# Performance work log

Measured on AMD Instinct MI355X. Metric: run time of the kernel, lower is better.

## Reference

```python
import jax, jax.numpy as jnp
import numpy as np

LAMBDA = 1.0          # lambda_param
SIGMA = 1.0           # RBF bandwidth (sigkernel convention: exp(-||x-y||^2 / sigma))
DYADIC_ORDER = 2
F = 2 ** DYADIC_ORDER # dyadic refinement factor per time axis

B, M_POP, DIM, SEQ_LEN = 4, 16, 8, 65


def _rbf_gram(X, Y):
    # X: (m, L, d), Y: (n, L, d) -> static kernel Gram (m, n, L, L)
    sx = jnp.sum(X * X, -1)                       # (m, L)
    sy = jnp.sum(Y * Y, -1)                       # (n, L)
    inner = jnp.einsum('isd,jtd->ijst', X, Y)     # (m, n, L, L)
    d2 = sx[:, None, :, None] + sy[None, :, None, :] - 2.0 * inner
    return jnp.exp(-d2 / SIGMA)


def _increments(G):
    # double increment of the static Gram over time, then dyadic refinement
    inc = G[..., 1:, 1:] + G[..., :-1, :-1] - G[..., 1:, :-1] - G[..., :-1, 1:]
    inc = jnp.repeat(jnp.repeat(inc, F, axis=-2), F, axis=-1) / (F * F)
    return inc  # (..., S, S) with S = F*(L-1)


def _solve_pde(M):
    # Goursat PDE explicit finite-difference scheme (as in sigkernel):
    # K[i+1,j+1] = (K[i+1,j]+K[i,j+1])*(1 + m/2 + m^2/12) - K[i,j]*(1 - m^2/12)
    dtype = M.dtype
    S = M.shape[0]

    def row_step(prev_row, m_row):
        def cell(k_left, inp):
            k00, k01, m = inp
            a = 1.0 + 0.5 * m + m * m * (1.0 / 12.0)
            b = 1.0 - m * m * (1.0 / 12.0)
            k_new = (k_left + k01) * a - k00 * b
            return k_new, k_new
        _, tail = jax.lax.scan(cell, jnp.asarray(1.0, dtype),
                               (prev_row[:-1], prev_row[1:], m_row))
        new_row = jnp.concatenate([jnp.ones((1,), dtype), tail])
        return new_row, None

    row0 = jnp.ones((S + 1,), dtype)
    last_row, _ = jax.lax.scan(row_step, row0, M)
    return last_row[-1]


def _gram_sig(X, Y):
    # signature kernel Gram matrix: X (m,L,d), Y (n,L,d) -> (m,n)
    Minc = _increments(_rbf_gram(X, Y))
    return jax.vmap(jax.vmap(_solve_pde))(Minc)


def setup_inputs() -> dict:
    key = jax.random.key(0)
    k1, k2 = jax.random.split(key)
    generated_samples = jax.random.normal(k1, (B, M_POP, DIM, SEQ_LEN), dtype=jnp.float32)
    real_sample = jax.random.normal(k2, (B, DIM, SEQ_LEN), dtype=jnp.float32)
    return {"generated_samples": generated_samples, "real_sample": real_sample}


def reference(generated_samples, real_sample):
    # generated_samples: (B, m, dim, L); real_sample: (B, dim, L)
    gen = jnp.swapaxes(generated_samples, -1, -2)          # (B, m, L, d)
    real = jnp.swapaxes(real_sample, -1, -2)[:, None]      # (B, 1, L, d)
    m = gen.shape[1]
    K_XX = jax.vmap(_gram_sig)(gen, gen)                   # (B, m, m)
    K_XY = jax.vmap(_gram_sig)(gen, real)                  # (B, m, 1)
    self_sim = (jnp.sum(K_XX, axis=(-1, -2))
                - jnp.trace(K_XX, axis1=-2, axis2=-1)) / (m * (m - 1))
    cross_sim = jnp.mean(K_XY, axis=(-1, -2))
    return jnp.mean(LAMBDA / 2.0 * self_sim - cross_sim)
```

## Files before the change

### kernel.cpp

```cpp
#include <hip/hip_runtime.h>


#define SEQ   65
#define DIMS  8
#define MPOP  16
#define NBATCH 4
#define NPAIR_XX 120
#define NBLOCKS (NBATCH*(NPAIR_XX + MPOP))
#define MST 67

__device__ __forceinline__ float wave_shr1(float x) {
    int xi = __builtin_bit_cast(int, x);
    int r  = __builtin_amdgcn_update_dpp(xi, xi, 0x138, 0xF, 0xF, false);
    return __builtin_bit_cast(float, r);
}
__device__ __forceinline__ float wave_shl1(float x) {
    int xi = __builtin_bit_cast(int, x);
    int r  = __builtin_amdgcn_update_dpp(xi, xi, 0x130, 0xF, 0xF, false);
    return __builtin_bit_cast(float, r);
}
__device__ __forceinline__ int clamp63(int v) {
    return v < 0 ? 0 : (v > 63 ? 63 : v);
}

__global__ __launch_bounds__(64, 1) void sigker_kernel(
    const float* __restrict__ gen,
    const float* __restrict__ realp,
    float* __restrict__ ws)
{
    __shared__ __align__(16) float YsF[SEQ * DIMS];
    __shared__ float R64[SEQ];
    __shared__ float MmL[64 * MST];

    const int tid = threadIdx.x;
    const int I   = tid;
    const int bid = blockIdx.x;

    int b, ii, jj; bool cross;
    if (bid < NBATCH * NPAIR_XX) {
        b = bid / NPAIR_XX;
        int p = bid % NPAIR_XX;
        int i = 0, acc = 0;
        while (p >= acc + (MPOP - 1 - i)) { acc += (MPOP - 1 - i); ++i; }
        ii = i; jj = i + 1 + (p - acc); cross = false;
    } else {
        int t = bid - NBATCH * NPAIR_XX;
        b = t / MPOP; ii = t % MPOP; jj = 0; cross = true;
    }

    const float* Xg = gen + (size_t)(b * MPOP + ii) * (DIMS * SEQ);
    const float* Yg = cross ? (realp + (size_t)b * (DIMS * SEQ))
                            : (gen + (size_t)(b * MPOP + jj) * (DIMS * SEQ));

    for (int f = tid; f < SEQ * DIMS; f += 64) {
        int d = f / SEQ, s = f - d * SEQ;
        YsF[s * DIMS + d] = Yg[f];
    }
    float x0[DIMS], x64[DIMS];
    #pragma unroll
    for (int d = 0; d < DIMS; ++d) {
        x0[d]  = Xg[d * SEQ + I];
        x64[d] = Xg[d * SEQ + 64];
    }
    __syncthreads();

    for (int t = tid; t < SEQ; t += 64) {
        const float4* yv = (const float4*)&YsF[t * DIMS];
        float4 ya = yv[0], yb = yv[1];
        float dd = 0.f;
        float a0;
        a0 = x64[0]-ya.x; dd += a0*a0;  a0 = x64[1]-ya.y; dd += a0*a0;
        a0 = x64[2]-ya.z; dd += a0*a0;  a0 = x64[3]-ya.w; dd += a0*a0;
        a0 = x64[4]-yb.x; dd += a0*a0;  a0 = x64[5]-yb.y; dd += a0*a0;
        a0 = x64[6]-yb.z; dd += a0*a0;  a0 = x64[7]-yb.w; dd += a0*a0;
        R64[t] = __expf(-dd);
    }
    __syncthreads();

    float* mrow = &MmL[I * MST];
    float ep, enp;
    {
        const float4* yv = (const float4*)&YsF[0];
        float4 ya = yv[0], yb = yv[1];
        float dd = 0.f, a0;
        a0 = x0[0]-ya.x; dd += a0*a0;  a0 = x0[1]-ya.y; dd += a0*a0;
        a0 = x0[2]-ya.z; dd += a0*a0;  a0 = x0[3]-ya.w; dd += a0*a0;
        a0 = x0[4]-yb.x; dd += a0*a0;  a0 = x0[5]-yb.y; dd += a0*a0;
        a0 = x0[6]-yb.z; dd += a0*a0;  a0 = x0[7]-yb.w; dd += a0*a0;
        float e  = __expf(-dd);
        float en = wave_shl1(e);
        float r  = R64[0];
        en = (I == 63) ? r : en;
        ep = e; enp = en;
    }
    #pragma unroll 4
    for (int t = 1; t < SEQ; ++t) {
        const float4* yv = (const float4*)&YsF[t * DIMS];
        float4 ya = yv[0], yb = yv[1];
        float dd = 0.f, a0;
        a0 = x0[0]-ya.x; dd += a0*a0;  a0 = x0[1]-ya.y; dd += a0*a0;
        a0 = x0[2]-ya.z; dd += a0*a0;  a0 = x0[3]-ya.w; dd += a0*a0;
        a0 = x0[4]-yb.x; dd += a0*a0;  a0 = x0[5]-yb.y; dd += a0*a0;
        a0 = x0[6]-yb.z; dd += a0*a0;  a0 = x0[7]-yb.w; dd += a0*a0;
        float e  = __expf(-dd);
        float en = wave_shl1(e);
        float r  = R64[t];
        en = (I == 63) ? r : en;
        mrow[t - 1] = ((en + ep) - (enp + e)) * (1.0f / 16.0f);
        ep = e; enp = en;
    }

    float l0 = 1.f, l1 = 1.f, l2 = 1.f, l3 = 1.f;
    float b0 = 1.f, b1 = 1.f, b2 = 1.f, b3 = 1.f;
    float cnext = 1.f;

#define STEP(DTv, MV) do {                                              \
        float t0_ = wave_shr1(b0);                                      \
        float t1_ = wave_shr1(b1);                                      \
        float t2_ = wave_shr1(b2);                                      \
        float t3_ = wave_shr1(b3);                                      \
        float cc_ = cnext; cnext = t3_;                                 \
        if (I == 0) { t0_ = t1_ = t2_ = t3_ = 1.f; cc_ = 1.f; }         \
        int J_ = (DTv) - I;                                             \
        if ((unsigned)J_ < 64u) {                                       \
            if (J_ == 0) cc_ = 1.f;                                     \
            float m_   = (MV);                                          \
            float q12_ = m_ * m_ * (1.0f / 12.0f);                      \
            float a_   = 1.0f + 0.5f * m_ + q12_;                       \
            float nb_  = q12_ - 1.0f;                                   \
            float u0_ = a_ * t0_ + nb_ * cc_;                           \
            float u1_ = a_ * t1_ + nb_ * t0_;                           \
            float u2_ = a_ * t2_ + nb_ * t1_;                           \
            float u3_ = a_ * t3_ + nb_ * t2_;                           \
            float q1_ = a_ * l0 + u0_;                                  \
            float q2_ = a_ * q1_ + u1_;                                 \
            float q3_ = a_ * q2_ + u2_;                                 \
            float q4_ = a_ * q3_ + u3_;                                 \
            u0_ = a_ * q1_ + nb_ * l0;  u1_ = a_ * q2_ + nb_ * q1_;     \
            u2_ = a_ * q3_ + nb_ * q2_; u3_ = a_ * q4_ + nb_ * q3_;     \
            float r1_ = a_ * l1 + u0_;                                  \
            float r2_ = a_ * r1_ + u1_;                                 \
            float r3_ = a_ * r2_ + u2_;                                 \
            float r4_ = a_ * r3_ + u3_;                                 \
            u0_ = a_ * r1_ + nb_ * l1;  u1_ = a_ * r2_ + nb_ * r1_;     \
            u2_ = a_ * r3_ + nb_ * r2_; u3_ = a_ * r4_ + nb_ * r3_;     \
            float s1_ = a_ * l2 + u0_;                                  \
            float s2_ = a_ * s1_ + u1_;                                 \
            float s3_ = a_ * s2_ + u2_;                                 \
            float s4_ = a_ * s3_ + u3_;                                 \
            u0_ = a_ * s1_ + nb_ * l2;  u1_ = a_ * s2_ + nb_ * s1_;     \
            u2_ = a_ * s3_ + nb_ * s2_; u3_ = a_ * s4_ + nb_ * s3_;     \
            float v1_ = a_ * l3 + u0_;                                  \
            float v2_ = a_ * v1_ + u1_;                                 \
            float v3_ = a_ * v2_ + u2_;                                 \
            float v4_ = a_ * v3_ + u3_;                                 \
            b0 = v1_; b1 = v2_; b2 = v3_; b3 = v4_;                     \
            l0 = q4_; l1 = r4_; l2 = s4_; l3 = v4_;                     \
        }                                                               \
    } while (0)

    float m0 = mrow[clamp63(0 - I)];
    float m1 = mrow[clamp63(1 - I)];
    float m2 = mrow[clamp63(2 - I)];
    float m3 = mrow[clamp63(3 - I)];

    for (int g = 0; g < 32; ++g) {
        const int DT0 = g * 4;
        float n0 = mrow[clamp63(DT0 + 4 - I)];
        float n1 = mrow[clamp63(DT0 + 5 - I)];
        float n2 = mrow[clamp63(DT0 + 6 - I)];
        float n3 = mrow[clamp63(DT0 + 7 - I)];
        STEP(DT0 + 0, m0);
        STEP(DT0 + 1, m1);
        STEP(DT0 + 2, m2);
        STEP(DT0 + 3, m3);
        m0 = n0; m1 = n1; m2 = n2; m3 = n3;
    }
#undef STEP

    if (tid == 63) {
        float w = cross ? (-1.0f / 32.0f) : (1.0f / 480.0f);
        ws[bid] = w * b3;
    }
}

__global__ __launch_bounds__(64, 1) void sigker_reduce(
    const float* __restrict__ ws, float* __restrict__ out)
{
    const int lane = threadIdx.x;
    float s = 0.f;
    for (int k = lane; k < NBLOCKS; k += 64) s += ws[k];
    #pragma unroll
    for (int off = 32; off >= 1; off >>= 1) s += __shfl_xor(s, off);
    if (lane == 0) out[0] = s;
}

extern "C" void kernel_launch(void* const* d_in, const int* in_sizes, int n_in,
                              void* d_out, int out_size, void* d_ws, size_t ws_size,
                              hipStream_t stream) {
    const float* gen   = (const float*)d_in[0];
    const float* realp = (const float*)d_in[1];
    if (n_in >= 2 && in_sizes[0] == NBATCH * DIMS * SEQ) {
        gen   = (const float*)d_in[1];
        realp = (const float*)d_in[0];
    }
    float* ws  = (float*)d_ws;
    float* out = (float*)d_out;
    sigker_kernel<<<NBLOCKS, 64, 0, stream>>>(gen, realp, ws);
    sigker_reduce<<<1, 64, 0, stream>>>(ws, out);
}
```

Baseline: 90.09 us.

## Remove branch from PDE wavefront via zero-padded skewed M layout

Stores each lane's increment row in a zero-padded, skewed shared buffer so the wavefront loop can read m with a fixed stride. This removes the per-step bounds check and the clamp indexing. Out-of-range cells see m=0, which makes the update act as identity on the boundary values. The loop becomes 127 unconditional steps with 8-deep prefetch. It also rewrites the RBF distance as norms minus twice the dot product, and adds a shared-memory zeroing pass plus a larger LDS footprint.

```diff
diff --git a/kernel.cpp b/kernel.cpp
--- a/kernel.cpp
+++ b/kernel.cpp
@@ -7,7 +7,7 @@
 #define NBATCH 4
 #define NPAIR_XX 120
 #define NBLOCKS (NBATCH*(NPAIR_XX + MPOP))
-#define MST 67
+#define MROW  194
 
 __device__ __forceinline__ float wave_shr1(float x) {
     int xi = __builtin_bit_cast(int, x);
@@ -18,9 +18,6 @@
     int xi = __builtin_bit_cast(int, x);
     int r  = __builtin_amdgcn_update_dpp(xi, xi, 0x130, 0xF, 0xF, false);
     return __builtin_bit_cast(float, r);
-}
-__device__ __forceinline__ int clamp63(int v) {
-    return v < 0 ? 0 : (v > 63 ? 63 : v);
 }
 
 __global__ __launch_bounds__(64, 1) void sigker_kernel(
@@ -30,11 +27,22 @@
 {
     __shared__ __align__(16) float YsF[SEQ * DIMS];
     __shared__ float R64[SEQ];
-    __shared__ float MmL[64 * MST];
+    __shared__ float YnL[SEQ];
+    __shared__ __align__(16) float MmL[64 * MROW];
 
     const int tid = threadIdx.x;
     const int I   = tid;
+    const bool lane0 = (I == 0);
     const int bid = blockIdx.x;
+
+    {
+        float4 z4 = make_float4(0.f, 0.f, 0.f, 0.f);
+        float4* M4 = (float4*)MmL;
+        #pragma unroll
+        for (int k = 0; k < (64 * MROW) / 4 / 64; ++k)
+            M4[k * 64 + tid] = z4;
+        if (tid < 32) M4[48 * 64 + tid] = z4;
+    }
 
     int b, ii, jj; bool cross;
     if (bid < NBATCH * NPAIR_XX) {
@@ -57,125 +65,115 @@
         YsF[s * DIMS + d] = Yg[f];
     }
     float x0[DIMS], x64[DIMS];
+    float xn0 = 0.f, xn64 = 0.f;
     #pragma unroll
     for (int d = 0; d < DIMS; ++d) {
         x0[d]  = Xg[d * SEQ + I];
         x64[d] = Xg[d * SEQ + 64];
+        xn0  += x0[d]  * x0[d];
+        xn64 += x64[d] * x64[d];
     }
     __syncthreads();
 
     for (int t = tid; t < SEQ; t += 64) {
         const float4* yv = (const float4*)&YsF[t * DIMS];
         float4 ya = yv[0], yb = yv[1];
-        float dd = 0.f;
-        float a0;
-        a0 = x64[0]-ya.x; dd += a0*a0;  a0 = x64[1]-ya.y; dd += a0*a0;
-        a0 = x64[2]-ya.z; dd += a0*a0;  a0 = x64[3]-ya.w; dd += a0*a0;
-        a0 = x64[4]-yb.x; dd += a0*a0;  a0 = x64[5]-yb.y; dd += a0*a0;
-        a0 = x64[6]-yb.z; dd += a0*a0;  a0 = x64[7]-yb.w; dd += a0*a0;
-        R64[t] = __expf(-dd);
+        float yn  = ya.x*ya.x + ya.y*ya.y + ya.z*ya.z + ya.w*ya.w
+                  + yb.x*yb.x + yb.y*yb.y + yb.z*yb.z + yb.w*yb.w;
+        float dot = x64[0]*ya.x + x64[1]*ya.y + x64[2]*ya.z + x64[3]*ya.w
+                  + x64[4]*yb.x + x64[5]*yb.y + x64[6]*yb.z + x64[7]*yb.w;
+        YnL[t] = yn;
+        R64[t] = __expf(2.f*dot - xn64 - yn);
     }
     __syncthreads();
 
-    float* mrow = &MmL[I * MST];
+    float* mrowW = &MmL[I * MROW + 64];
     float ep, enp;
     {
         const float4* yv = (const float4*)&YsF[0];
         float4 ya = yv[0], yb = yv[1];
-        float dd = 0.f, a0;
-        a0 = x0[0]-ya.x; dd += a0*a0;  a0 = x0[1]-ya.y; dd += a0*a0;
-        a0 = x0[2]-ya.z; dd += a0*a0;  a0 = x0[3]-ya.w; dd += a0*a0;
-        a0 = x0[4]-yb.x; dd += a0*a0;  a0 = x0[5]-yb.y; dd += a0*a0;
-        a0 = x0[6]-yb.z; dd += a0*a0;  a0 = x0[7]-yb.w; dd += a0*a0;
-        float e  = __expf(-dd);
+        float dot = x0[0]*ya.x + x0[1]*ya.y + x0[2]*ya.z + x0[3]*ya.w
+                  + x0[4]*yb.x + x0[5]*yb.y + x0[6]*yb.z + x0[7]*yb.w;
+        float e  = __expf(2.f*dot - xn0 - YnL[0]);
         float en = wave_shl1(e);
-        float r  = R64[0];
-        en = (I == 63) ? r : en;
+        en = (I == 63) ? R64[0] : en;
         ep = e; enp = en;
     }
     #pragma unroll 4
     for (int t = 1; t < SEQ; ++t) {
         const float4* yv = (const float4*)&YsF[t * DIMS];
         float4 ya = yv[0], yb = yv[1];
-        float dd = 0.f, a0;
-        a0 = x0[0]-ya.x; dd += a0*a0;  a0 = x0[1]-ya.y; dd += a0*a0;
-        a0 = x0[2]-ya.z; dd += a0*a0;  a0 = x0[3]-ya.w; dd += a0*a0;
-        a0 = x0[4]-yb.x; dd += a0*a0;  a0 = x0[5]-yb.y; dd += a0*a0;
-        a0 = x0[6]-yb.z; dd += a0*a0;  a0 = x0[7]-yb.w; dd += a0*a0;
-        float e  = __expf(-dd);
+        float dot = x0[0]*ya.x + x0[1]*ya.y + x0[2]*ya.z + x0[3]*ya.w
+                  + x0[4]*yb.x + x0[5]*yb.y + x0[6]*yb.z + x0[7]*yb.w;
+        float e  = __expf(2.f*dot - xn0 - YnL[t]);
         float en = wave_shl1(e);
-        float r  = R64[t];
-        en = (I == 63) ? r : en;
-        mrow[t - 1] = ((en + ep) - (enp + e)) * (1.0f / 16.0f);
+        en = (I == 63) ? R64[t] : en;
+        mrowW[t - 1] = ((en - enp) + (ep - e)) * (1.0f / 16.0f);
         ep = e; enp = en;
     }
 
+    const float* mpde = &MmL[193 * I + 64];
     float l0 = 1.f, l1 = 1.f, l2 = 1.f, l3 = 1.f;
     float b0 = 1.f, b1 = 1.f, b2 = 1.f, b3 = 1.f;
     float cnext = 1.f;
 
-#define STEP(DTv, MV) do {                                              \
+#define STEP(MV) do {                                                   \
         float t0_ = wave_shr1(b0);                                      \
         float t1_ = wave_shr1(b1);                                      \
         float t2_ = wave_shr1(b2);                                      \
         float t3_ = wave_shr1(b3);                                      \
+        if (lane0) { t0_ = 1.f; t1_ = 1.f; t2_ = 1.f; t3_ = 1.f; }      \
         float cc_ = cnext; cnext = t3_;                                 \
-        if (I == 0) { t0_ = t1_ = t2_ = t3_ = 1.f; cc_ = 1.f; }         \
-        int J_ = (DTv) - I;                                             \
-        if ((unsigned)J_ < 64u) {                                       \
-            if (J_ == 0) cc_ = 1.f;                                     \
-            float m_   = (MV);                                          \
-            float q12_ = m_ * m_ * (1.0f / 12.0f);                      \
-            float a_   = 1.0f + 0.5f * m_ + q12_;                       \
-            float nb_  = q12_ - 1.0f;                                   \
-            float u0_ = a_ * t0_ + nb_ * cc_;                           \
-            float u1_ = a_ * t1_ + nb_ * t0_;                           \
-            float u2_ = a_ * t2_ + nb_ * t1_;                           \
-            float u3_ = a_ * t3_ + nb_ * t2_;                           \
-            float q1_ = a_ * l0 + u0_;                                  \
-            float q2_ = a_ * q1_ + u1_;                                 \
-            float q3_ = a_ * q2_ + u2_;                                 \
-            float q4_ = a_ * q3_ + u3_;                                 \
-            u0_ = a_ * q1_ + nb_ * l0;  u1_ = a_ * q2_ + nb_ * q1_;     \
-            u2_ = a_ * q3_ + nb_ * q2_; u3_ = a_ * q4_ + nb_ * q3_;     \
-            float r1_ = a_ * l1 + u0_;                                  \
-            float r2_ = a_ * r1_ + u1_;                                 \
-            float r3_ = a_ * r2_ + u2_;                                 \
-            float r4_ = a_ * r3_ + u3_;                                 \
-            u0_ = a_ * r1_ + nb_ * l1;  u1_ = a_ * r2_ + nb_ * r1_;     \
-            u2_ = a_ * r3_ + nb_ * r2_; u3_ = a_ * r4_ + nb_ * r3_;     \
-            float s1_ = a_ * l2 + u0_;                                  \
-            float s2_ = a_ * s1_ + u1_;                                 \
-            float s3_ = a_ * s2_ + u2_;                                 \
-            float s4_ = a_ * s3_ + u3_;                                 \
-            u0_ = a_ * s1_ + nb_ * l2;  u1_ = a_ * s2_ + nb_ * s1_;     \
-            u2_ = a_ * s3_ + nb_ * s2_; u3_ = a_ * s4_ + nb_ * s3_;     \
-            float v1_ = a_ * l3 + u0_;                                  \
-            float v2_ = a_ * v1_ + u1_;                                 \
-            float v3_ = a_ * v2_ + u2_;                                 \
-            float v4_ = a_ * v3_ + u3_;                                 \
-            b0 = v1_; b1 = v2_; b2 = v3_; b3 = v4_;                     \
-            l0 = q4_; l1 = r4_; l2 = s4_; l3 = v4_;                     \
-        }                                                               \
+        float m_   = (MV);                                              \
+        float q12_ = m_ * m_ * (1.0f / 12.0f);                          \
+        float a_   = 1.0f + 0.5f * m_ + q12_;                           \
+        float nb_  = q12_ - 1.0f;                                       \
+        float u0_ = a_ * t0_ + nb_ * cc_;                               \
+        float u1_ = a_ * t1_ + nb_ * t0_;                               \
+        float u2_ = a_ * t2_ + nb_ * t1_;                               \
+        float u3_ = a_ * t3_ + nb_ * t2_;                               \
+        float q1_ = a_ * l0 + u0_;                                      \
+        float q2_ = a_ * q1_ + u1_;                                     \
+        float q3_ = a_ * q2_ + u2_;                                     \
+        float q4_ = a_ * q3_ + u3_;                                     \
+        u0_ = a_ * q1_ + nb_ * l0;  u1_ = a_ * q2_ + nb_ * q1_;         \
+        u2_ = a_ * q3_ + nb_ * q2_; u3_ = a_ * q4_ + nb_ * q3_;         \
+        float r1_ = a_ * l1 + u0_;                                      \
+        float r2_ = a_ * r1_ + u1_;                                     \
+        float r3_ = a_ * r2_ + u2_;                                     \
+        float r4_ = a_ * r3_ + u3_;                                     \
+        u0_ = a_ * r1_ + nb_ * l1;  u1_ = a_ * r2_ + nb_ * r1_;         \
+        u2_ = a_ * r3_ + nb_ * r2_; u3_ = a_ * r4_ + nb_ * r3_;         \
+        float s1_ = a_ * l2 + u0_;                                      \
+        float s2_ = a_ * s1_ + u1_;                                     \
+        float s3_ = a_ * s2_ + u2_;                                     \
+        float s4_ = a_ * s3_ + u3_;                                     \
+        u0_ = a_ * s1_ + nb_ * l2;  u1_ = a_ * s2_ + nb_ * s1_;         \
+        u2_ = a_ * s3_ + nb_ * s2_; u3_ = a_ * s4_ + nb_ * s3_;         \
+        float v1_ = a_ * l3 + u0_;                                      \
+        float v2_ = a_ * v1_ + u1_;                                     \
+        float v3_ = a_ * v2_ + u2_;                                     \
+        float v4_ = a_ * v3_ + u3_;                                     \
+        b0 = v1_; b1 = v2_; b2 = v3_; b3 = v4_;                         \
+        l0 = q4_; l1 = r4_; l2 = s4_; l3 = v4_;                         \
     } while (0)
 
-    float m0 = mrow[clamp63(0 - I)];
-    float m1 = mrow[clamp63(1 - I)];
-    float m2 = mrow[clamp63(2 - I)];
-    float m3 = mrow[clamp63(3 - I)];
-
-    for (int g = 0; g < 32; ++g) {
-        const int DT0 = g * 4;
-        float n0 = mrow[clamp63(DT0 + 4 - I)];
-        float n1 = mrow[clamp63(DT0 + 5 - I)];
-        float n2 = mrow[clamp63(DT0 + 6 - I)];
-        float n3 = mrow[clamp63(DT0 + 7 - I)];
-        STEP(DT0 + 0, m0);
-        STEP(DT0 + 1, m1);
-        STEP(DT0 + 2, m2);
-        STEP(DT0 + 3, m3);
+    float m0 = mpde[0], m1 = mpde[1], m2 = mpde[2], m3 = mpde[3];
+    float m4 = mpde[4], m5 = mpde[5], m6 = mpde[6], m7 = mpde[7];
+
+    for (int g = 0; g < 15; ++g) {
+        const int nb_ = (g + 1) * 8;
+        float n0 = mpde[nb_ + 0], n1 = mpde[nb_ + 1];
+        float n2 = mpde[nb_ + 2], n3 = mpde[nb_ + 3];
+        float n4 = mpde[nb_ + 4], n5 = mpde[nb_ + 5];
+        float n6 = mpde[nb_ + 6], n7 = mpde[nb_ + 7];
+        STEP(m0); STEP(m1); STEP(m2); STEP(m3);
+        STEP(m4); STEP(m5); STEP(m6); STEP(m7);
         m0 = n0; m1 = n1; m2 = n2; m3 = n3;
-    }
+        m4 = n4; m5 = n5; m6 = n6; m7 = n7;
+    }
+    STEP(m0); STEP(m1); STEP(m2); STEP(m3);
+    STEP(m4); STEP(m5); STEP(m6);
 #undef STEP
 
     if (tid == 63) {
```

Measured after the change: 85.59 us. -5.0%, faster.
